# Kernel optimization log

Hardware: AMD Instinct MI355X
Metric: run time of the kernel (lower is better)

The kernel has to match this reference:

```python
import jax, jax.numpy as jnp
import numpy as np

N, E, B, PG = 20000, 320000, 20, 1000  # nodes, edges, graphs, nodes-per-graph
H, L, NB, EI = 256, 6, 16, 8           # hidden, layers, node_base_dim, edge_in_dim
LN_EPS = 1e-5


def setup_inputs() -> dict:
    key = jax.random.key(0)
    ks = jax.random.split(key, 32)
    w = lambda i, s: (jax.random.normal(ks[i], s, jnp.float32) * 0.05)
    inp = {
        "x": jax.random.normal(ks[0], (N, NB), jnp.float32),
        "edge_attr": jax.random.normal(ks[1], (E, EI), jnp.float32),
        "c": jax.random.normal(ks[2], (B, PG), jnp.float32),
        "edge_index": jax.random.randint(ks[3], (2, E), 0, N),
        "node_gid": jnp.arange(N) // PG,   # batch.batch
        "node_lid": jnp.arange(N) % PG,    # node local index
        # edge_mlp: Linear(EI,H), ReLU, Linear(H,H)
        "ew1": w(4, (EI, H)), "eb1": jnp.zeros((H,), jnp.float32),
        "ew2": w(5, (H, H)),  "eb2": jnp.zeros((H,), jnp.float32),
        # input_proj: Linear(NB+1, H), SiLU
        "in_w": w(6, (NB + 1, H)), "in_b": jnp.zeros((H,), jnp.float32),
        # per-layer GINEConv edge lin (edge_dim -> in_channels)
        "lin_w": w(7, (L, H, H)), "lin_b": jnp.zeros((L, H), jnp.float32),
        # per-layer conv MLP: Linear(H,H), SiLU, Linear(H,H)
        "cw1": w(8, (L, H, H)), "cb1": jnp.zeros((L, H), jnp.float32),
        "cw2": w(9, (L, H, H)), "cb2": jnp.zeros((L, H), jnp.float32),
        # per-layer LayerNorm
        "ln_g": jnp.ones((L, H), jnp.float32), "ln_b": jnp.zeros((L, H), jnp.float32),
        # pool_attn: Linear(H,H), Tanh, Linear(H,1)
        "pa_w1": w(10, (H, H)), "pa_b1": jnp.zeros((H,), jnp.float32),
        "pa_w2": w(11, (H, 1)), "pa_b2": jnp.zeros((1,), jnp.float32),
        # head: Linear(H,H), SiLU, Linear(H,1)
        "hw1": w(12, (H, H)), "hb1": jnp.zeros((H,), jnp.float32),
        "hw2": w(13, (H, 1)), "hb2": jnp.zeros((1,), jnp.float32),
    }
    return inp


def _layer_norm(z, g, b):
    m = jnp.mean(z, axis=-1, keepdims=True)
    v = jnp.mean(jnp.square(z - m), axis=-1, keepdims=True)
    return (z - m) * jax.lax.rsqrt(v + LN_EPS) * g + b


def reference(x, edge_attr, c, edge_index, node_gid, node_lid,
              ew1, eb1, ew2, eb2, in_w, in_b,
              lin_w, lin_b, cw1, cb1, cw2, cb2, ln_g, ln_b,
              pa_w1, pa_b1, pa_w2, pa_b2, hw1, hb1, hw2, hb2):
    silu = jax.nn.silu
    # c_scalar: per-node coefficient
    c_scalar = c[node_gid, node_lid][:, None]                       # [N,1]
    xin = jnp.concatenate([x, c_scalar], axis=-1)                   # [N,NB+1]
    e = jax.nn.relu(edge_attr @ ew1 + eb1) @ ew2 + eb2              # [E,H]
    h = silu(xin @ in_w + in_b)                                     # [N,H]
    src, dst = edge_index[0], edge_index[1]
    for l in range(L):
        msg = jax.nn.relu(h[src] + (e @ lin_w[l] + lin_b[l]))       # [E,H]
        agg = jnp.zeros_like(h).at[dst].add(msg)                    # scatter-add
        z = h + agg                                                 # (1+eps)*x_i + agg, eps=0
        h_new = silu(z @ cw1[l] + cb1[l]) @ cw2[l] + cb2[l]
        h_new = _layer_norm(h_new, ln_g[l], ln_b[l])
        h = h + silu(h_new)
    # attention pooling: global softmax over nodes, renormalized per graph
    scores = jnp.tanh(h @ pa_w1 + pa_b1) @ pa_w2 + pa_b2            # [N,1]
    attn = jax.nn.softmax(scores, axis=0)                           # [N,1]
    seg_sum = jax.ops.segment_sum(attn[:, 0], node_gid, num_segments=B)  # [B]
    attn_n = attn[:, 0] / (seg_sum[node_gid] + 1e-8)                # [N]
    pooled = jax.ops.segment_sum(h * attn_n[:, None], node_gid, num_segments=B)  # [B,H]
    q = (silu(pooled @ hw1 + hb1) @ hw2 + hb2)[:, 0]                # [B]
    return q
```

## Files before the change

### kernel.cpp

```cpp
#include <hip/hip_runtime.h>
#include <hip/hip_bf16.h>
#include <cstdint>


#define NN 20000
#define EE 320000
#define BBG 20
#define PGN 1000
#define HH 256
#define LL 6

typedef short bf16x8 __attribute__((ext_vector_type(8)));
typedef float f32x4 __attribute__((ext_vector_type(4)));

__device__ __forceinline__ void async16(const void* g, void* l) {
  __builtin_amdgcn_global_load_lds(
      (const __attribute__((address_space(1))) unsigned int*)(uintptr_t)g,
      (__attribute__((address_space(3))) unsigned int*)(uintptr_t)l, 16, 0, 0);
}

__device__ __forceinline__ float siluf(float x) { return x / (1.f + __expf(-x)); }

__device__ __forceinline__ unsigned int f2bu(float x) {
  __hip_bfloat16 h = __float2bfloat16(x);
  return (unsigned int)*(unsigned short*)&h;
}

__device__ __forceinline__ float b2f(unsigned short u) {
  unsigned int v = ((unsigned int)u) << 16;
  return *(float*)&v;
}

enum { EPI_SILU = 1, EPI_PLAIN = 2, EPI_TANH = 3 };

template <int EPI>
__global__ void __launch_bounds__(256, 2) gemm256(
    const __hip_bfloat16* __restrict__ A, const __hip_bfloat16* __restrict__ Wt,
    const float* __restrict__ bias, int M, float* __restrict__ outf,
    __hip_bfloat16* __restrict__ outb) {
  __shared__ __align__(16) __hip_bfloat16 sA[128 * 32];
  __shared__ __align__(16) __hip_bfloat16 sB[128 * 32];

  const int t = threadIdx.x;
  const int wave = t >> 6, lane = t & 63;
  const int row0 = blockIdx.x * 128;
  const int col0 = blockIdx.y * 128;

  const int wrow = (wave >> 1) * 64;
  const int wcol = (wave & 1) * 64;
  const int fr = lane & 15, q = lane >> 4;

  f32x4 zero = {0.f, 0.f, 0.f, 0.f};
  f32x4 acc[4][4];
#pragma unroll
  for (int i = 0; i < 4; i++)
#pragma unroll
    for (int j = 0; j < 4; j++) acc[i][j] = zero;

  const int c1 = t, c2 = t + 256;
  const int lr1 = c1 >> 2, lr2 = c2 >> 2;
  const int q1 = (c1 & 3) ^ ((lr1 >> 1) & 3);
  const int q2 = (c2 & 3) ^ ((lr2 >> 1) & 3);
  int rA1 = row0 + lr1; if (rA1 >= M) rA1 = M - 1;
  int rA2 = row0 + lr2; if (rA2 >= M) rA2 = M - 1;
  const int rB1 = col0 + lr1, rB2 = col0 + lr2;

  for (int k0 = 0; k0 < 256; k0 += 32) {
    async16((const char*)(A + (size_t)rA1 * HH + k0) + q1 * 16,
            (char*)sA + wave * 1024);
    async16((const char*)(A + (size_t)rA2 * HH + k0) + q2 * 16,
            (char*)sA + 4096 + wave * 1024);
    async16((const char*)(Wt + (size_t)rB1 * HH + k0) + q1 * 16,
            (char*)sB + wave * 1024);
    async16((const char*)(Wt + (size_t)rB2 * HH + k0) + q2 * 16,
            (char*)sB + 4096 + wave * 1024);
    __syncthreads();
    bf16x8 af[4], bfr[4];
#pragma unroll
    for (int i = 0; i < 4; i++) {
      const int row = wrow + i * 16 + fr;
      af[i] = *(const bf16x8*)&sA[row * 32 + ((q ^ ((row >> 1) & 3))) * 8];
    }
#pragma unroll
    for (int j = 0; j < 4; j++) {
      const int row = wcol + j * 16 + fr;
      bfr[j] = *(const bf16x8*)&sB[row * 32 + ((q ^ ((row >> 1) & 3))) * 8];
    }
#pragma unroll
    for (int i = 0; i < 4; i++)
#pragma unroll
      for (int j = 0; j < 4; j++)
        acc[i][j] = __builtin_amdgcn_mfma_f32_16x16x32_bf16(af[i], bfr[j],
                                                            acc[i][j], 0, 0, 0);
    __syncthreads();
  }

#pragma unroll
  for (int j = 0; j < 4; j++) {
    const int col = col0 + wcol + j * 16 + fr;
    const float bs = bias[col];
#pragma unroll
    for (int i = 0; i < 4; i++) {
      const int lr0 = wrow + i * 16 + q * 4;
#pragma unroll
      for (int r = 0; r < 4; r++) {
        const int grow = row0 + lr0 + r;
        float v = acc[i][j][r] + bs;
        if (grow < M) {
          if (EPI == EPI_SILU) {
            outb[(size_t)grow * HH + col] = __float2bfloat16(siluf(v));
          } else if (EPI == EPI_PLAIN) {
            outf[(size_t)grow * HH + col] = v;
          } else {
            outb[(size_t)grow * HH + col] = __float2bfloat16(tanhf(v));
          }
        }
      }
    }
  }
}

__global__ void __launch_bounds__(256, 2) gemm_silu_f32(
    const float* __restrict__ A, const __hip_bfloat16* __restrict__ Wt,
    const float* __restrict__ bias, int M, __hip_bfloat16* __restrict__ outb) {
  __shared__ __align__(16) __hip_bfloat16 sA[128 * 32];
  __shared__ __align__(16) __hip_bfloat16 sB[128 * 32];

  const int t = threadIdx.x;
  const int wave = t >> 6, lane = t & 63;
  const int row0 = blockIdx.x * 128;
  const int col0 = blockIdx.y * 128;

  const int wrow = (wave >> 1) * 64;
  const int wcol = (wave & 1) * 64;
  const int fr = lane & 15, q = lane >> 4;

  f32x4 zero = {0.f, 0.f, 0.f, 0.f};
  f32x4 acc[4][4];
#pragma unroll
  for (int i = 0; i < 4; i++)
#pragma unroll
    for (int j = 0; j < 4; j++) acc[i][j] = zero;

  const int c1 = t, c2 = t + 256;
  const int lr1 = c1 >> 2, lr2 = c2 >> 2;
  const int q1 = (c1 & 3) ^ ((lr1 >> 1) & 3);
  const int q2 = (c2 & 3) ^ ((lr2 >> 1) & 3);
  int rA1 = row0 + lr1; if (rA1 >= M) rA1 = M - 1;
  int rA2 = row0 + lr2; if (rA2 >= M) rA2 = M - 1;
  const int rB1 = col0 + lr1, rB2 = col0 + lr2;

  for (int k0 = 0; k0 < 256; k0 += 32) {
    async16((const char*)(Wt + (size_t)rB1 * HH + k0) + q1 * 16,
            (char*)sB + wave * 1024);
    async16((const char*)(Wt + (size_t)rB2 * HH + k0) + q2 * 16,
            (char*)sB + 4096 + wave * 1024);
    {
      const float* s1 = A + (size_t)rA1 * HH + k0 + q1 * 8;
      float4 a0 = *(const float4*)s1;
      float4 a1 = *(const float4*)(s1 + 4);
      uint4 u;
      u.x = f2bu(a0.x) | (f2bu(a0.y) << 16);
      u.y = f2bu(a0.z) | (f2bu(a0.w) << 16);
      u.z = f2bu(a1.x) | (f2bu(a1.y) << 16);
      u.w = f2bu(a1.z) | (f2bu(a1.w) << 16);
      *(uint4*)((char*)sA + wave * 1024 + lane * 16) = u;
    }
    {
      const float* s2 = A + (size_t)rA2 * HH + k0 + q2 * 8;
      float4 a0 = *(const float4*)s2;
      float4 a1 = *(const float4*)(s2 + 4);
      uint4 u;
      u.x = f2bu(a0.x) | (f2bu(a0.y) << 16);
      u.y = f2bu(a0.z) | (f2bu(a0.w) << 16);
      u.z = f2bu(a1.x) | (f2bu(a1.y) << 16);
      u.w = f2bu(a1.z) | (f2bu(a1.w) << 16);
      *(uint4*)((char*)sA + 4096 + wave * 1024 + lane * 16) = u;
    }
    __syncthreads();
    bf16x8 af[4], bfr[4];
#pragma unroll
    for (int i = 0; i < 4; i++) {
      const int row = wrow + i * 16 + fr;
      af[i] = *(const bf16x8*)&sA[row * 32 + ((q ^ ((row >> 1) & 3))) * 8];
    }
#pragma unroll
    for (int j = 0; j < 4; j++) {
      const int row = wcol + j * 16 + fr;
      bfr[j] = *(const bf16x8*)&sB[row * 32 + ((q ^ ((row >> 1) & 3))) * 8];
    }
#pragma unroll
    for (int i = 0; i < 4; i++)
#pragma unroll
      for (int j = 0; j < 4; j++)
        acc[i][j] = __builtin_amdgcn_mfma_f32_16x16x32_bf16(af[i], bfr[j],
                                                            acc[i][j], 0, 0, 0);
    __syncthreads();
  }

#pragma unroll
  for (int j = 0; j < 4; j++) {
    const int col = col0 + wcol + j * 16 + fr;
    const float bs = bias[col];
#pragma unroll
    for (int i = 0; i < 4; i++) {
      const int lr0 = wrow + i * 16 + q * 4;
#pragma unroll
      for (int r = 0; r < 4; r++) {
        const int grow = row0 + lr0 + r;
        if (grow < M)
          outb[(size_t)grow * HH + col] =
              __float2bfloat16(siluf(acc[i][j][r] + bs));
      }
    }
  }
}

__global__ void __launch_bounds__(256, 2) gemm_ln(
    const __hip_bfloat16* __restrict__ A, const __hip_bfloat16* __restrict__ Wt,
    const float* __restrict__ bias, const float* __restrict__ g,
    const float* __restrict__ bbv, float* __restrict__ h,
    float* __restrict__ yzf, __hip_bfloat16* __restrict__ hb) {
  __shared__ __align__(16) char smem[64 * 264 * 2];
  __hip_bfloat16* sA = (__hip_bfloat16*)smem;
  __hip_bfloat16* sB = (__hip_bfloat16*)(smem + 4096);
  unsigned short* yb = (unsigned short*)smem;

  const int t = threadIdx.x;
  const int wave = t >> 6, lane = t & 63;
  const int row0 = blockIdx.x * 64;
  const int wrow = (wave >> 1) * 32;
  const int wcol = (wave & 1) * 128;
  const int fr = lane & 15, q = lane >> 4;

  f32x4 zero = {0.f, 0.f, 0.f, 0.f};
  f32x4 acc[2][8];
#pragma unroll
  for (int i = 0; i < 2; i++)
#pragma unroll
    for (int j = 0; j < 8; j++) acc[i][j] = zero;

  const int lrA = t >> 2;
  const int qA = (t & 3) ^ ((lrA >> 1) & 3);
  int rA = row0 + lrA; if (rA >= NN) rA = NN - 1;
  int qB[4], rB[4];
#pragma unroll
  for (int p = 0; p < 4; p++) {
    const int c = t + p * 256;
    const int lr = c >> 2;
    qB[p] = (c & 3) ^ ((lr >> 1) & 3);
    rB[p] = lr;
  }

  for (int k0 = 0; k0 < 256; k0 += 32) {
    async16((const char*)(A + (size_t)rA * HH + k0) + qA * 16,
            (char*)sA + wave * 1024);
#pragma unroll
    for (int p = 0; p < 4; p++)
      async16((const char*)(Wt + (size_t)rB[p] * HH + k0) + qB[p] * 16,
              (char*)sB + p * 4096 + wave * 1024);
    __syncthreads();
    bf16x8 af[2], bfr[8];
#pragma unroll
    for (int i = 0; i < 2; i++) {
      const int row = wrow + i * 16 + fr;
      af[i] = *(const bf16x8*)&sA[row * 32 + ((q ^ ((row >> 1) & 3))) * 8];
    }
#pragma unroll
    for (int j = 0; j < 8; j++) {
      const int row = wcol + j * 16 + fr;
      bfr[j] = *(const bf16x8*)&sB[row * 32 + ((q ^ ((row >> 1) & 3))) * 8];
    }
#pragma unroll
    for (int i = 0; i < 2; i++)
#pragma unroll
      for (int j = 0; j < 8; j++)
        acc[i][j] = __builtin_amdgcn_mfma_f32_16x16x32_bf16(af[i], bfr[j],
                                                            acc[i][j], 0, 0, 0);
    __syncthreads();
  }

#pragma unroll
  for (int j = 0; j < 8; j++) {
    const int col = wcol + j * 16 + fr;
    const float bs = bias[col];
#pragma unroll
    for (int i = 0; i < 2; i++) {
      const int r0 = wrow + i * 16 + q * 4;
#pragma unroll
      for (int r = 0; r < 4; r++)
        yb[(r0 + r) * 264 + col] = (unsigned short)f2bu(acc[i][j][r] + bs);
    }
  }
  __syncthreads();

  for (int rr = 0; rr < 16; rr++) {
    const int r = wave * 16 + rr;
    const int grow = row0 + r;
    if (grow >= NN) break;
    float v[4];
    float s = 0.f;
#pragma unroll
    for (int i = 0; i < 4; i++) {
      v[i] = b2f(yb[r * 264 + lane + i * 64]);
      s += v[i];
    }
#pragma unroll
    for (int o = 32; o; o >>= 1) s += __shfl_xor(s, o);
    const float mean = s * (1.f / 256.f);
    float var = 0.f;
#pragma unroll
    for (int i = 0; i < 4; i++) { float d = v[i] - mean; var += d * d; }
#pragma unroll
    for (int o = 32; o; o >>= 1) var += __shfl_xor(var, o);
    const float rs = rsqrtf(var * (1.f / 256.f) + 1e-5f);
#pragma unroll
    for (int i = 0; i < 4; i++) {
      const int c = lane + i * 64;
      float ln = (v[i] - mean) * rs * g[c] + bbv[c];
      float si = siluf(ln);
      size_t idx = (size_t)grow * HH + c;
      float nh = h[idx] + si;
      h[idx] = nh;
      yzf[idx] = nh;
      hb[idx] = __float2bfloat16(nh);
    }
  }
}

__global__ void __launch_bounds__(256, 3) edge_fused(
    const __hip_bfloat16* __restrict__ te, const __hip_bfloat16* __restrict__ Wt,
    const float* __restrict__ bias, const __hip_bfloat16* __restrict__ hbv,
    const int* __restrict__ srcp, const int* __restrict__ dstp,
    float* __restrict__ z) {
  __shared__ __align__(16) char smem[32768];
  __shared__ int sSrc[128], sDst[128];
  __hip_bfloat16* sA = (__hip_bfloat16*)smem;
  __hip_bfloat16* sB = (__hip_bfloat16*)(smem + 16384);
  unsigned short* sRed = (unsigned short*)smem;

  const int t = threadIdx.x;
  const int wave = t >> 6, lane = t & 63;
  const int row0 = blockIdx.y * 128;
  const int col0 = blockIdx.x * 128;

  if (t < 128) { sSrc[t] = srcp[row0 + t]; sDst[t] = dstp[row0 + t]; }
  __syncthreads();

  const int wrow = (wave >> 1) * 64;
  const int fr = lane & 15, q = lane >> 4;
  const int rc = lane, rb = wave;

  f32x4 zero = {0.f, 0.f, 0.f, 0.f};
  f32x4 acc[4][4];
#pragma unroll
  for (int i = 0; i < 4; i++)
#pragma unroll
    for (int j = 0; j < 4; j++) acc[i][j] = zero;

  const int c1 = t, c2 = t + 256;
  const int lr1 = c1 >> 2, lr2 = c2 >> 2;
  const int q1 = (c1 & 3) ^ ((lr1 >> 1) & 3);
  const int q2 = (c2 & 3) ^ ((lr2 >> 1) & 3);
  const int rA1 = row0 + lr1, rA2 = row0 + lr2;
  const int rB1 = col0 + lr1, rB2 = col0 + lr2;

  float hv[32];

#pragma unroll
  for (int it = 0; it < 4; it++) {
    const int ka = it * 64, kb = ka + 32;
    async16((const char*)(te + (size_t)rA1 * HH + ka) + q1 * 16,
            (char*)sA + wave * 1024);
    async16((const char*)(te + (size_t)rA2 * HH + ka) + q2 * 16,
            (char*)sA + 4096 + wave * 1024);
    async16((const char*)(te + (size_t)rA1 * HH + kb) + q1 * 16,
            (char*)sA + 8192 + wave * 1024);
    async16((const char*)(te + (size_t)rA2 * HH + kb) + q2 * 16,
            (char*)sA + 12288 + wave * 1024);
    async16((const char*)(Wt + (size_t)rB1 * HH + ka) + q1 * 16,
            (char*)sB + wave * 1024);
    async16((const char*)(Wt + (size_t)rB2 * HH + ka) + q2 * 16,
            (char*)sB + 4096 + wave * 1024);
    async16((const char*)(Wt + (size_t)rB1 * HH + kb) + q1 * 16,
            (char*)sB + 8192 + wave * 1024);
    async16((const char*)(Wt + (size_t)rB2 * HH + kb) + q2 * 16,
            (char*)sB + 12288 + wave * 1024);
#pragma unroll
    for (int u = 0; u < 8; u++) {
      const int r = it * 8 + u;
      hv[r] = __bfloat162float(hbv[(size_t)sSrc[rb * 32 + r] * HH + col0 + rc]);
    }
    __syncthreads();
#pragma unroll
    for (int half = 0; half < 2; half++) {
      const __hip_bfloat16* pA = sA + half * 4096;
      const __hip_bfloat16* pB = sB + half * 4096;
      bf16x8 af[4], bfr[4];
#pragma unroll
      for (int i = 0; i < 4; i++) {
        const int row = wrow + i * 16 + fr;
        af[i] = *(const bf16x8*)&pA[row * 32 + ((q ^ ((row >> 1) & 3))) * 8];
      }
#pragma unroll
      for (int j = 0; j < 4; j++) {
        const int row = (wave & 1) * 64 + j * 16 + fr;
        bfr[j] = *(const bf16x8*)&pB[row * 32 + ((q ^ ((row >> 1) & 3))) * 8];
      }
#pragma unroll
      for (int i = 0; i < 4; i++)
#pragma unroll
        for (int j = 0; j < 4; j++)
          acc[i][j] = __builtin_amdgcn_mfma_f32_16x16x32_bf16(af[i], bfr[j],
                                                              acc[i][j], 0, 0, 0);
    }
    __syncthreads();
  }

#pragma unroll
  for (int hf = 0; hf < 2; hf++) {
    if ((wave & 1) == hf) {
#pragma unroll
      for (int j = 0; j < 4; j++) {
        const int cl = j * 16 + fr;
        const float bs = bias[col0 + hf * 64 + cl];
#pragma unroll
        for (int i = 0; i < 4; i++) {
          const int r0 = wrow + i * 16 + q * 4;
          f32x4 v = acc[i][j];
          unsigned int p0 = f2bu(v[0] + bs) | (f2bu(v[1] + bs) << 16);
          unsigned int p1 = f2bu(v[2] + bs) | (f2bu(v[3] + bs) << 16);
          *(unsigned int*)&sRed[cl * 130 + r0] = p0;
          *(unsigned int*)&sRed[cl * 130 + r0 + 2] = p1;
        }
      }
    }
    __syncthreads();
    const int gcol = col0 + hf * 64 + rc;
    float a = 0.f;
    int cur = sDst[rb * 32];
#pragma unroll 4
    for (int rr = 0; rr < 32; rr++) {
      const int row = rb * 32 + rr;
      const int d = sDst[row];
      if (d != cur) {
        unsafeAtomicAdd(&z[(size_t)cur * HH + gcol], a);
        a = 0.f;
        cur = d;
      }
      float m = b2f(sRed[rc * 130 + row]) + hv[rr];
      a += m > 0.f ? m : 0.f;
    }
    unsafeAtomicAdd(&z[(size_t)cur * HH + gcol], a);
    if (hf == 0) {
#pragma unroll
      for (int rr = 0; rr < 32; rr++)
        hv[rr] = __bfloat162float(
            hbv[(size_t)sSrc[rb * 32 + rr] * HH + col0 + 64 + rc]);
    }
    __syncthreads();
  }
}

__global__ void __launch_bounds__(256) hist_k(const int* __restrict__ edst,
                                              int* __restrict__ cnt) {
  const int e = blockIdx.x * 256 + threadIdx.x;
  if (e < EE) atomicAdd(&cnt[edst[e]], 1);
}

__global__ void __launch_bounds__(256) scan_k(const int* __restrict__ cnt,
                                              int* __restrict__ rowptr) {
  __shared__ int buf[256];
  __shared__ int carry;
  const int t = threadIdx.x;
  if (t == 0) carry = 0;
  __syncthreads();
  for (int base = 0; base < NN; base += 256) {
    const int idx = base + t;
    int v = (idx < NN) ? cnt[idx] : 0;
    buf[t] = v;
    __syncthreads();
    for (int o = 1; o < 256; o <<= 1) {
      int x = (t >= o) ? buf[t - o] : 0;
      __syncthreads();
      buf[t] += x;
      __syncthreads();
    }
    if (idx < NN) rowptr[idx] = carry + buf[t] - v;
    __syncthreads();
    if (t == 255) carry += buf[255];
    __syncthreads();
  }
  if (t == 0) rowptr[NN] = carry;
}

__global__ void __launch_bounds__(256) scatter_k(
    const int* __restrict__ esrc, const int* __restrict__ edst,
    int* __restrict__ cursor, int* __restrict__ posof,
    int* __restrict__ srcp, int* __restrict__ dstp) {
  const int e = blockIdx.x * 256 + threadIdx.x;
  if (e < EE) {
    const int d = edst[e];
    const int pos = atomicAdd(&cursor[d], 1);
    posof[e] = pos;
    srcp[pos] = esrc[e];
    dstp[pos] = d;
  }
}

__global__ void __launch_bounds__(256) edge_hidden(
    const float* __restrict__ ea, const float* __restrict__ ew1,
    const float* __restrict__ eb1, const int* __restrict__ posof,
    __hip_bfloat16* __restrict__ tout) {
  __shared__ float w[8 * 256];
  __shared__ float b[256];
  __shared__ float sea[16 * 8];
  __shared__ int spos[16];
  const int t = threadIdx.x;
  for (int i = t; i < 8 * 256; i += 256) w[i] = ew1[i];
  b[t] = eb1[t];
  const int e0 = blockIdx.x * 16;
  if (t < 128) sea[t] = ea[(size_t)e0 * 8 + t];
  if (t < 16) spos[t] = posof[e0 + t];
  __syncthreads();
  for (int e = 0; e < 16; e++) {
    float a = b[t];
#pragma unroll
    for (int j = 0; j < 8; j++) a += sea[e * 8 + j] * w[j * 256 + t];
    tout[(size_t)spos[e] * HH + t] = __float2bfloat16(a > 0.f ? a : 0.f);
  }
}

__global__ void __launch_bounds__(256) fold_edge_w(
    const float* __restrict__ ew2, const float* __restrict__ lin_w,
    const float* __restrict__ eb2, const float* __restrict__ lin_b,
    __hip_bfloat16* __restrict__ Wlt, float* __restrict__ bl) {
  const int l = blockIdx.x >> 8, j = blockIdx.x & 255;
  const int c = threadIdx.x;
  __shared__ float row[256];
  row[c] = ew2[j * 256 + c];
  __syncthreads();
  const float* lw = lin_w + (size_t)l * 65536;
  float a = 0.f;
  for (int k = 0; k < 256; k++) a += row[k] * lw[k * 256 + c];
  Wlt[((size_t)l * 256 + c) * 256 + j] = __float2bfloat16(a);
  if (j == 0) {
    float s = lin_b[l * 256 + c];
    for (int k = 0; k < 256; k++) s += eb2[k] * lw[k * 256 + c];
    bl[l * 256 + c] = s;
  }
}

__global__ void __launch_bounds__(256) tcast_all(
    const float* __restrict__ cw1, const float* __restrict__ cw2,
    const float* __restrict__ paw1, __hip_bfloat16* __restrict__ cw1t,
    __hip_bfloat16* __restrict__ cw2t, __hip_bfloat16* __restrict__ paw1t) {
  const int b = blockIdx.x;
  const float* s;
  __hip_bfloat16* d;
  if (b < 1536) { int l = b >> 8; s = cw1 + (size_t)l * 65536; d = cw1t + (size_t)l * 65536; }
  else if (b < 3072) { int l = (b - 1536) >> 8; s = cw2 + (size_t)l * 65536; d = cw2t + (size_t)l * 65536; }
  else { s = paw1; d = paw1t; }
  const int r = b & 255, c = threadIdx.x;
  d[(size_t)c * 256 + r] = __float2bfloat16(s[(size_t)r * 256 + c]);
}

__global__ void __launch_bounds__(256) node_init(
    const float* __restrict__ x, const float* __restrict__ cc,
    const int* __restrict__ gid, const int* __restrict__ lid,
    const float* __restrict__ in_w, const float* __restrict__ in_b,
    float* __restrict__ h, float* __restrict__ yzf,
    __hip_bfloat16* __restrict__ hb) {
  __shared__ float w[17 * 256];
  __shared__ float b[256];
  __shared__ float sx[16 * 17];
  const int t = threadIdx.x;
  for (int i = t; i < 17 * 256; i += 256) w[i] = in_w[i];
  b[t] = in_b[t];
  const int n0 = blockIdx.x * 16;
  sx[(t >> 4) * 17 + (t & 15)] = x[(size_t)(n0 + (t >> 4)) * 16 + (t & 15)];
  if (t < 16) {
    int n = n0 + t;
    sx[t * 17 + 16] = cc[gid[n] * PGN + lid[n]];
  }
  __syncthreads();
  for (int e = 0; e < 16; e++) {
    float a = b[t];
#pragma unroll
    for (int j = 0; j < 17; j++) a += sx[e * 17 + j] * w[j * 256 + t];
    float s = siluf(a);
    size_t idx = (size_t)(n0 + e) * HH + t;
    h[idx] = s;
    yzf[idx] = s;
    hb[idx] = __float2bfloat16(s);
  }
}

__global__ void __launch_bounds__(256) score_k(
    const __hip_bfloat16* __restrict__ s1, const float* __restrict__ pw2,
    const float* __restrict__ pb2, float* __restrict__ scores,
    float* __restrict__ pmax) {
  __shared__ float w2[256];
  __shared__ float bm[4];
  const int t = threadIdx.x, wave = t >> 6, lane = t & 63;
  w2[t] = pw2[t];
  __syncthreads();
  const size_t row = (size_t)blockIdx.x * 4 + wave;
  float a = 0.f;
#pragma unroll
  for (int i = 0; i < 4; i++) {
    int c = lane + i * 64;
    a += __bfloat162float(s1[row * HH + c]) * w2[c];
  }
#pragma unroll
  for (int o = 32; o; o >>= 1) a += __shfl_xor(a, o);
  float sc = a + pb2[0];
  if (lane == 0) { scores[row] = sc; bm[wave] = sc; }
  __syncthreads();
  if (t == 0) pmax[blockIdx.x] = fmaxf(fmaxf(bm[0], bm[1]), fmaxf(bm[2], bm[3]));
}

__global__ void __launch_bounds__(256) gmax_k(const float* __restrict__ pmax,
                                              int n, float* __restrict__ gmax) {
  const int t = threadIdx.x;
  float m = -3.4e38f;
  for (int i = t; i < n; i += 256) m = fmaxf(m, pmax[i]);
#pragma unroll
  for (int o = 32; o; o >>= 1) m = fmaxf(m, __shfl_xor(m, o));
  __shared__ float wm[4];
  if ((t & 63) == 0) wm[t >> 6] = m;
  __syncthreads();
  if (t == 0) gmax[0] = fmaxf(fmaxf(wm[0], wm[1]), fmaxf(wm[2], wm[3]));
}

__global__ void __launch_bounds__(256) esum_k(
    const float* __restrict__ scores, const int* __restrict__ gid,
    const float* __restrict__ gmax, float* __restrict__ en,
    float* __restrict__ seg) {
  __shared__ float ls[BBG + 1];
  const int t = threadIdx.x;
  if (t < BBG + 1) ls[t] = 0.f;
  __syncthreads();
  const int n = blockIdx.x * 256 + t;
  if (n < NN) {
    float e = __expf(scores[n] - gmax[0]);
    en[n] = e;
    atomicAdd(&ls[gid[n]], e);
    atomicAdd(&ls[BBG], e);
  }
  __syncthreads();
  if (t < BBG + 1) unsafeAtomicAdd(&seg[t], ls[t]);
}

__global__ void __launch_bounds__(256) pooled_k(
    const float* __restrict__ h, const float* __restrict__ en,
    const float* __restrict__ seg, float* __restrict__ pooled) {
  const int g = blockIdx.x / 40, ch = blockIdx.x % 40;
  const int c = threadIdx.x;
  const int n0 = g * PGN + ch * 25;
  float a = 0.f;
  for (int i = 0; i < 25; i++) {
    int n = n0 + i;
    a += en[n] * h[(size_t)n * HH + c];
  }
  const float inv = 1.f / (seg[g] + 1e-8f * seg[BBG]);
  unsafeAtomicAdd(&pooled[g * HH + c], a * inv);
}

__global__ void __launch_bounds__(256) head_k(
    const float* __restrict__ pooled, const float* __restrict__ hw1,
    const float* __restrict__ hb1, const float* __restrict__ hw2,
    const float* __restrict__ hb2, float* __restrict__ qout) {
  const int b = blockIdx.x, c = threadIdx.x;
  __shared__ float p[256];
  __shared__ float wsum[4];
  p[c] = pooled[b * 256 + c];
  __syncthreads();
  float a = hb1[c];
  for (int k = 0; k < 256; k++) a += p[k] * hw1[k * 256 + c];
  float v = siluf(a) * hw2[c];
#pragma unroll
  for (int o = 32; o; o >>= 1) v += __shfl_xor(v, o);
  if ((c & 63) == 0) wsum[c >> 6] = v;
  __syncthreads();
  if (c == 0) qout[b] = wsum[0] + wsum[1] + wsum[2] + wsum[3] + hb2[0];
}

extern "C" void kernel_launch(void* const* d_in, const int* in_sizes, int n_in,
                              void* d_out, int out_size, void* d_ws, size_t ws_size,
                              hipStream_t stream) {
  const float* x = (const float*)d_in[0];
  const float* edge_attr = (const float*)d_in[1];
  const float* cc = (const float*)d_in[2];
  const int* edge_index = (const int*)d_in[3];
  const int* node_gid = (const int*)d_in[4];
  const int* node_lid = (const int*)d_in[5];
  const float* ew1 = (const float*)d_in[6];
  const float* eb1 = (const float*)d_in[7];
  const float* ew2 = (const float*)d_in[8];
  const float* eb2 = (const float*)d_in[9];
  const float* in_w = (const float*)d_in[10];
  const float* in_b = (const float*)d_in[11];
  const float* lin_w = (const float*)d_in[12];
  const float* lin_b = (const float*)d_in[13];
  const float* cw1 = (const float*)d_in[14];
  const float* cb1 = (const float*)d_in[15];
  const float* cw2 = (const float*)d_in[16];
  const float* cb2 = (const float*)d_in[17];
  const float* ln_g = (const float*)d_in[18];
  const float* ln_b = (const float*)d_in[19];
  const float* pa_w1 = (const float*)d_in[20];
  const float* pa_b1 = (const float*)d_in[21];
  const float* pa_w2 = (const float*)d_in[22];
  const float* pa_b2 = (const float*)d_in[23];
  const float* hw1 = (const float*)d_in[24];
  const float* hb1 = (const float*)d_in[25];
  const float* hw2 = (const float*)d_in[26];
  const float* hb2 = (const float*)d_in[27];
  float* qout = (float*)d_out;

  char* w = (char*)d_ws;
  auto alloc = [&](size_t bytes) {
    char* p = w;
    w += (bytes + 255) & ~(size_t)255;
    return p;
  };
  __hip_bfloat16* t_e = (__hip_bfloat16*)alloc((size_t)EE * HH * 2);
  float* h = (float*)alloc((size_t)NN * HH * 4);
  float* yzf = (float*)alloc((size_t)NN * HH * 4);
  __hip_bfloat16* hb = (__hip_bfloat16*)alloc((size_t)NN * HH * 2);
  __hip_bfloat16* t2 = (__hip_bfloat16*)alloc((size_t)NN * HH * 2);
  __hip_bfloat16* Wlt = (__hip_bfloat16*)alloc((size_t)LL * HH * HH * 2);
  float* bl = (float*)alloc((size_t)LL * HH * 4);
  __hip_bfloat16* cw1t = (__hip_bfloat16*)alloc((size_t)LL * HH * HH * 2);
  __hip_bfloat16* cw2t = (__hip_bfloat16*)alloc((size_t)LL * HH * HH * 2);
  __hip_bfloat16* paw1t = (__hip_bfloat16*)alloc((size_t)HH * HH * 2);
  float* scores = (float*)alloc((size_t)NN * 4);
  float* pmax = (float*)alloc(5008 * 4);
  float* en = (float*)alloc((size_t)NN * 4);
  float* seg = (float*)alloc((BBG + 1) * 4);
  float* gmax = (float*)alloc(4);
  float* pooled = (float*)alloc((size_t)BBG * HH * 4);
  int* cnt = (int*)alloc((size_t)NN * 4);
  int* rowptr = (int*)alloc((size_t)(NN + 1) * 4);
  int* cursor = (int*)alloc((size_t)NN * 4);
  int* posof = (int*)alloc((size_t)EE * 4);
  int* srcp = (int*)alloc((size_t)EE * 4);
  int* dstp = (int*)alloc((size_t)EE * 4);

  const int* esrc = edge_index;
  const int* edst = edge_index + EE;

  hipMemsetAsync(cnt, 0, (size_t)NN * 4, stream);
  hipMemsetAsync(seg, 0, (BBG + 1) * 4, stream);
  hipMemsetAsync(pooled, 0, (size_t)BBG * HH * 4, stream);

  hist_k<<<(EE + 255) / 256, 256, 0, stream>>>(edst, cnt);
  scan_k<<<1, 256, 0, stream>>>(cnt, rowptr);
  hipMemcpyAsync(cursor, rowptr, (size_t)NN * 4, hipMemcpyDeviceToDevice, stream);
  scatter_k<<<(EE + 255) / 256, 256, 0, stream>>>(esrc, edst, cursor, posof,
                                                  srcp, dstp);

  fold_edge_w<<<LL * 256, 256, 0, stream>>>(ew2, lin_w, eb2, lin_b, Wlt, bl);
  tcast_all<<<3328, 256, 0, stream>>>(cw1, cw2, pa_w1, cw1t, cw2t, paw1t);
  edge_hidden<<<EE / 16, 256, 0, stream>>>(edge_attr, ew1, eb1, posof, t_e);
  node_init<<<NN / 16, 256, 0, stream>>>(x, cc, node_gid, node_lid, in_w, in_b,
                                         h, yzf, hb);

  dim3 gE(2, EE / 128), gN((NN + 127) / 128, 2);
  const int gLN = (NN + 63) / 64;
  for (int l = 0; l < LL; l++) {
    edge_fused<<<gE, 256, 0, stream>>>(t_e, Wlt + (size_t)l * HH * HH,
                                       bl + l * HH, hb, srcp, dstp, yzf);
    gemm_silu_f32<<<gN, 256, 0, stream>>>(
        yzf, cw1t + (size_t)l * HH * HH, cb1 + l * HH, NN, t2);
    gemm_ln<<<gLN, 256, 0, stream>>>(t2, cw2t + (size_t)l * HH * HH,
                                     cb2 + l * HH, ln_g + l * HH, ln_b + l * HH,
                                     h, yzf, hb);
  }

  gemm256<EPI_TANH><<<gN, 256, 0, stream>>>(hb, paw1t, pa_b1, NN, nullptr, t2);
  score_k<<<NN / 4, 256, 0, stream>>>(t2, pa_w2, pa_b2, scores, pmax);
  gmax_k<<<1, 256, 0, stream>>>(pmax, NN / 4, gmax);
  esum_k<<<(NN + 255) / 256, 256, 0, stream>>>(scores, node_gid, gmax, en, seg);
  pooled_k<<<BBG * 40, 256, 0, stream>>>(h, en, seg, pooled);
  head_k<<<BBG, 256, 0, stream>>>(pooled, hw1, hb1, hw2, hb2, qout);
}
```

Measured before the change: 1.377 ms.

## Recompute edge hidden features inside edge kernel instead of materializing them

Drops the precomputed [E,256] bf16 edge-hidden tensor. Each edge_fused block now rebuilds its A tile on the fly from the 8-wide raw edge attributes and ew1/eb1 held in shared memory, so every layer avoids reading a large buffer from global memory. In exchange, each block redoes the small 8-input matmul plus ReLU for every layer and column block, and shared-memory use and register pressure in the hot kernel go up. Separately, the one-block prefix scan now uses wave shuffles in place of a shared-memory Hillis-Steele loop with many barriers.

```diff
diff --git a/kernel.cpp b/kernel.cpp
--- a/kernel.cpp
+++ b/kernel.cpp
@@ -329,11 +329,14 @@
 }
 
 __global__ void __launch_bounds__(256, 3) edge_fused(
-    const __hip_bfloat16* __restrict__ te, const __hip_bfloat16* __restrict__ Wt,
-    const float* __restrict__ bias, const __hip_bfloat16* __restrict__ hbv,
-    const int* __restrict__ srcp, const int* __restrict__ dstp,
-    float* __restrict__ z) {
+    const float* __restrict__ ea, const int* __restrict__ eorig,
+    const float* __restrict__ ew1f, const float* __restrict__ eb1f,
+    const __hip_bfloat16* __restrict__ Wt, const float* __restrict__ bias,
+    const __hip_bfloat16* __restrict__ hbv, const int* __restrict__ srcp,
+    const int* __restrict__ dstp, float* __restrict__ z) {
   __shared__ __align__(16) char smem[32768];
+  __shared__ __align__(16) float sew1[8 * 256];
+  __shared__ float seb1[256];
   __shared__ int sSrc[128], sDst[128];
   __hip_bfloat16* sA = (__hip_bfloat16*)smem;
   __hip_bfloat16* sB = (__hip_bfloat16*)(smem + 16384);
@@ -345,11 +348,26 @@
   const int col0 = blockIdx.x * 128;
 
   if (t < 128) { sSrc[t] = srcp[row0 + t]; sDst[t] = dstp[row0 + t]; }
-  __syncthreads();
+  for (int i = t; i < 8 * 256; i += 256) sew1[i] = ew1f[i];
+  seb1[t] = eb1f[t];
+
+  const int rr = (t >> 3) * 4;
+  const int cc = (t & 7) * 4;
+  float ar[4][8];
+#pragma unroll
+  for (int i = 0; i < 4; i++) {
+    const int e = eorig[row0 + rr + i];
+    const float4 a0 = *(const float4*)&ea[(size_t)e * 8];
+    const float4 a1 = *(const float4*)&ea[(size_t)e * 8 + 4];
+    ar[i][0] = a0.x; ar[i][1] = a0.y; ar[i][2] = a0.z; ar[i][3] = a0.w;
+    ar[i][4] = a1.x; ar[i][5] = a1.y; ar[i][6] = a1.z; ar[i][7] = a1.w;
+  }
 
   const int wrow = (wave >> 1) * 64;
   const int fr = lane & 15, q = lane >> 4;
   const int rc = lane, rb = wave;
+  const int gch = cc >> 3;
+  const int hby = (cc & 7) * 2;
 
   f32x4 zero = {0.f, 0.f, 0.f, 0.f};
   f32x4 acc[4][4];
@@ -362,22 +380,15 @@
   const int lr1 = c1 >> 2, lr2 = c2 >> 2;
   const int q1 = (c1 & 3) ^ ((lr1 >> 1) & 3);
   const int q2 = (c2 & 3) ^ ((lr2 >> 1) & 3);
-  const int rA1 = row0 + lr1, rA2 = row0 + lr2;
   const int rB1 = col0 + lr1, rB2 = col0 + lr2;
 
   float hv[32];
+
+  __syncthreads();
 
 #pragma unroll
   for (int it = 0; it < 4; it++) {
     const int ka = it * 64, kb = ka + 32;
-    async16((const char*)(te + (size_t)rA1 * HH + ka) + q1 * 16,
-            (char*)sA + wave * 1024);
-    async16((const char*)(te + (size_t)rA2 * HH + ka) + q2 * 16,
-            (char*)sA + 4096 + wave * 1024);
-    async16((const char*)(te + (size_t)rA1 * HH + kb) + q1 * 16,
-            (char*)sA + 8192 + wave * 1024);
-    async16((const char*)(te + (size_t)rA2 * HH + kb) + q2 * 16,
-            (char*)sA + 12288 + wave * 1024);
     async16((const char*)(Wt + (size_t)rB1 * HH + ka) + q1 * 16,
             (char*)sB + wave * 1024);
     async16((const char*)(Wt + (size_t)rB2 * HH + ka) + q2 * 16,
@@ -386,6 +397,38 @@
             (char*)sB + 8192 + wave * 1024);
     async16((const char*)(Wt + (size_t)rB2 * HH + kb) + q2 * 16,
             (char*)sB + 12288 + wave * 1024);
+#pragma unroll
+    for (int half = 0; half < 2; half++) {
+      const int k0 = ka + half * 32;
+      float tv[4][4];
+      const float4 bb = *(const float4*)&seb1[k0 + cc];
+#pragma unroll
+      for (int i = 0; i < 4; i++) {
+        tv[i][0] = bb.x; tv[i][1] = bb.y; tv[i][2] = bb.z; tv[i][3] = bb.w;
+      }
+#pragma unroll
+      for (int j = 0; j < 8; j++) {
+        const float4 ww = *(const float4*)&sew1[j * 256 + k0 + cc];
+#pragma unroll
+        for (int i = 0; i < 4; i++) {
+          tv[i][0] += ar[i][j] * ww.x;
+          tv[i][1] += ar[i][j] * ww.y;
+          tv[i][2] += ar[i][j] * ww.z;
+          tv[i][3] += ar[i][j] * ww.w;
+        }
+      }
+#pragma unroll
+      for (int i = 0; i < 4; i++) {
+        const int r = rr + i;
+        const int sl = gch ^ ((r >> 1) & 3);
+        ushort4 pk;
+        pk.x = (unsigned short)f2bu(tv[i][0] > 0.f ? tv[i][0] : 0.f);
+        pk.y = (unsigned short)f2bu(tv[i][1] > 0.f ? tv[i][1] : 0.f);
+        pk.z = (unsigned short)f2bu(tv[i][2] > 0.f ? tv[i][2] : 0.f);
+        pk.w = (unsigned short)f2bu(tv[i][3] > 0.f ? tv[i][3] : 0.f);
+        *(ushort4*)((char*)sA + half * 8192 + r * 64 + sl * 16 + hby) = pk;
+      }
+    }
 #pragma unroll
     for (int u = 0; u < 8; u++) {
       const int r = it * 8 + u;
@@ -440,23 +483,23 @@
     float a = 0.f;
     int cur = sDst[rb * 32];
 #pragma unroll 4
-    for (int rr = 0; rr < 32; rr++) {
-      const int row = rb * 32 + rr;
+    for (int r2 = 0; r2 < 32; r2++) {
+      const int row = rb * 32 + r2;
       const int d = sDst[row];
       if (d != cur) {
         unsafeAtomicAdd(&z[(size_t)cur * HH + gcol], a);
         a = 0.f;
         cur = d;
       }
-      float m = b2f(sRed[rc * 130 + row]) + hv[rr];
+      float m = b2f(sRed[rc * 130 + row]) + hv[r2];
       a += m > 0.f ? m : 0.f;
     }
     unsafeAtomicAdd(&z[(size_t)cur * HH + gcol], a);
     if (hf == 0) {
 #pragma unroll
-      for (int rr = 0; rr < 32; rr++)
-        hv[rr] = __bfloat162float(
-            hbv[(size_t)sSrc[rb * 32 + rr] * HH + col0 + 64 + rc]);
+      for (int r2 = 0; r2 < 32; r2++)
+        hv[r2] = __bfloat162float(
+            hbv[(size_t)sSrc[rb * 32 + r2] * HH + col0 + 64 + rc]);
     }
     __syncthreads();
   }
@@ -470,25 +513,28 @@
 
 __global__ void __launch_bounds__(256) scan_k(const int* __restrict__ cnt,
                                               int* __restrict__ rowptr) {
-  __shared__ int buf[256];
+  __shared__ int wsum[4];
   __shared__ int carry;
-  const int t = threadIdx.x;
+  const int t = threadIdx.x, wave = t >> 6, lane = t & 63;
   if (t == 0) carry = 0;
   __syncthreads();
   for (int base = 0; base < NN; base += 256) {
     const int idx = base + t;
     int v = (idx < NN) ? cnt[idx] : 0;
-    buf[t] = v;
-    __syncthreads();
-    for (int o = 1; o < 256; o <<= 1) {
-      int x = (t >= o) ? buf[t - o] : 0;
-      __syncthreads();
-      buf[t] += x;
-      __syncthreads();
-    }
-    if (idx < NN) rowptr[idx] = carry + buf[t] - v;
-    __syncthreads();
-    if (t == 255) carry += buf[255];
+    int inc = v;
+#pragma unroll
+    for (int o = 1; o < 64; o <<= 1) {
+      int u = __shfl_up(inc, o);
+      if (lane >= o) inc += u;
+    }
+    if (lane == 63) wsum[wave] = inc;
+    __syncthreads();
+    int woff = 0;
+    for (int w2 = 0; w2 < wave; w2++) woff += wsum[w2];
+    if (idx < NN) rowptr[idx] = carry + woff + inc - v;
+    const int total = wsum[0] + wsum[1] + wsum[2] + wsum[3];
+    __syncthreads();
+    if (t == 0) carry += total;
     __syncthreads();
   }
   if (t == 0) rowptr[NN] = carry;
@@ -496,38 +542,15 @@
 
 __global__ void __launch_bounds__(256) scatter_k(
     const int* __restrict__ esrc, const int* __restrict__ edst,
-    int* __restrict__ cursor, int* __restrict__ posof,
+    int* __restrict__ cursor, int* __restrict__ eorig,
     int* __restrict__ srcp, int* __restrict__ dstp) {
   const int e = blockIdx.x * 256 + threadIdx.x;
   if (e < EE) {
     const int d = edst[e];
     const int pos = atomicAdd(&cursor[d], 1);
-    posof[e] = pos;
+    eorig[pos] = e;
     srcp[pos] = esrc[e];
     dstp[pos] = d;
-  }
-}
-
-__global__ void __launch_bounds__(256) edge_hidden(
-    const float* __restrict__ ea, const float* __restrict__ ew1,
-    const float* __restrict__ eb1, const int* __restrict__ posof,
-    __hip_bfloat16* __restrict__ tout) {
-  __shared__ float w[8 * 256];
-  __shared__ float b[256];
-  __shared__ float sea[16 * 8];
-  __shared__ int spos[16];
-  const int t = threadIdx.x;
-  for (int i = t; i < 8 * 256; i += 256) w[i] = ew1[i];
-  b[t] = eb1[t];
-  const int e0 = blockIdx.x * 16;
-  if (t < 128) sea[t] = ea[(size_t)e0 * 8 + t];
-  if (t < 16) spos[t] = posof[e0 + t];
-  __syncthreads();
-  for (int e = 0; e < 16; e++) {
-    float a = b[t];
-#pragma unroll
-    for (int j = 0; j < 8; j++) a += sea[e * 8 + j] * w[j * 256 + t];
-    tout[(size_t)spos[e] * HH + t] = __float2bfloat16(a > 0.f ? a : 0.f);
   }
 }
 
@@ -725,7 +748,6 @@
     w += (bytes + 255) & ~(size_t)255;
     return p;
   };
-  __hip_bfloat16* t_e = (__hip_bfloat16*)alloc((size_t)EE * HH * 2);
   float* h = (float*)alloc((size_t)NN * HH * 4);
   float* yzf = (float*)alloc((size_t)NN * HH * 4);
   __hip_bfloat16* hb = (__hip_bfloat16*)alloc((size_t)NN * HH * 2);
@@ -744,7 +766,7 @@
   int* cnt = (int*)alloc((size_t)NN * 4);
   int* rowptr = (int*)alloc((size_t)(NN + 1) * 4);
   int* cursor = (int*)alloc((size_t)NN * 4);
-  int* posof = (int*)alloc((size_t)EE * 4);
+  int* eorig = (int*)alloc((size_t)EE * 4);
   int* srcp = (int*)alloc((size_t)EE * 4);
   int* dstp = (int*)alloc((size_t)EE * 4);
 
@@ -758,20 +780,20 @@
   hist_k<<<(EE + 255) / 256, 256, 0, stream>>>(edst, cnt);
   scan_k<<<1, 256, 0, stream>>>(cnt, rowptr);
   hipMemcpyAsync(cursor, rowptr, (size_t)NN * 4, hipMemcpyDeviceToDevice, stream);
-  scatter_k<<<(EE + 255) / 256, 256, 0, stream>>>(esrc, edst, cursor, posof,
+  scatter_k<<<(EE + 255) / 256, 256, 0, stream>>>(esrc, edst, cursor, eorig,
                                                   srcp, dstp);
 
   fold_edge_w<<<LL * 256, 256, 0, stream>>>(ew2, lin_w, eb2, lin_b, Wlt, bl);
   tcast_all<<<3328, 256, 0, stream>>>(cw1, cw2, pa_w1, cw1t, cw2t, paw1t);
-  edge_hidden<<<EE / 16, 256, 0, stream>>>(edge_attr, ew1, eb1, posof, t_e);
   node_init<<<NN / 16, 256, 0, stream>>>(x, cc, node_gid, node_lid, in_w, in_b,
                                          h, yzf, hb);
 
   dim3 gE(2, EE / 128), gN((NN + 127) / 128, 2);
   const int gLN = (NN + 63) / 64;
   for (int l = 0; l < LL; l++) {
-    edge_fused<<<gE, 256, 0, stream>>>(t_e, Wlt + (size_t)l * HH * HH,
-                                       bl + l * HH, hb, srcp, dstp, yzf);
+    edge_fused<<<gE, 256, 0, stream>>>(edge_attr, eorig, ew1, eb1,
+                                       Wlt + (size_t)l * HH * HH, bl + l * HH,
+                                       hb, srcp, dstp, yzf);
     gemm_silu_f32<<<gN, 256, 0, stream>>>(
         yzf, cw1t + (size_t)l * HH * HH, cb1 + l * HH, NN, t2);
     gemm_ln<<<gLN, 256, 0, stream>>>(t2, cw2t + (size_t)l * HH * HH,
```

New measurement: 1.808 ms. 31.3% more time.

## Fuse conv MLP GEMMs with LayerNorm and restructure edge gather and scan

Applied to the files above, without the earlier changes.

Merges the two per-layer conv MLP GEMMs and the LayerNorm into one kernel. The SiLU intermediate for each 64-row tile stays in shared memory as bf16 instead of going through global memory. The edge kernel now gathers h[src] in chunks of 8 just before accumulation rather than holding a 32-float register array, and its launch bound rises to 4 blocks. The single-block scan switches to wave shuffles. The fused kernel uses more shared memory and gives each wave all 256 columns, which may lower occupancy and reuse.

```diff
diff --git a/kernel.cpp b/kernel.cpp
--- a/kernel.cpp
+++ b/kernel.cpp
@@ -120,43 +120,43 @@
   }
 }
 
-__global__ void __launch_bounds__(256, 2) gemm_silu_f32(
-    const float* __restrict__ A, const __hip_bfloat16* __restrict__ Wt,
-    const float* __restrict__ bias, int M, __hip_bfloat16* __restrict__ outb) {
-  __shared__ __align__(16) __hip_bfloat16 sA[128 * 32];
-  __shared__ __align__(16) __hip_bfloat16 sB[128 * 32];
+__global__ void __launch_bounds__(256, 2) mlp_ln(
+    const float* __restrict__ z, const __hip_bfloat16* __restrict__ W1t,
+    const float* __restrict__ b1, const __hip_bfloat16* __restrict__ W2t,
+    const float* __restrict__ b2, const float* __restrict__ g,
+    const float* __restrict__ bbv, float* __restrict__ h,
+    float* __restrict__ yzf, __hip_bfloat16* __restrict__ hb) {
+  __shared__ __align__(16) char smem[20480 + 64 * 264 * 2];
+  __hip_bfloat16* sA = (__hip_bfloat16*)smem;
+  __hip_bfloat16* sB = (__hip_bfloat16*)(smem + 4096);
+  unsigned short* sT = (unsigned short*)(smem + 20480);
 
   const int t = threadIdx.x;
   const int wave = t >> 6, lane = t & 63;
-  const int row0 = blockIdx.x * 128;
-  const int col0 = blockIdx.y * 128;
-
-  const int wrow = (wave >> 1) * 64;
-  const int wcol = (wave & 1) * 64;
+  const int row0 = blockIdx.x * 64;
   const int fr = lane & 15, q = lane >> 4;
+  const int wr = wave * 16;
+
+  const int lrA = t >> 2;
+  const int qA = (t & 3) ^ ((lrA >> 1) & 3);
+  int rA = row0 + lrA; if (rA >= NN) rA = NN - 1;
+  int qB[4], rB[4];
+#pragma unroll
+  for (int p = 0; p < 4; p++) {
+    const int c = t + p * 256;
+    const int lr = c >> 2;
+    qB[p] = (c & 3) ^ ((lr >> 1) & 3);
+    rB[p] = lr;
+  }
 
   f32x4 zero = {0.f, 0.f, 0.f, 0.f};
-  f32x4 acc[4][4];
-#pragma unroll
-  for (int i = 0; i < 4; i++)
-#pragma unroll
-    for (int j = 0; j < 4; j++) acc[i][j] = zero;
-
-  const int c1 = t, c2 = t + 256;
-  const int lr1 = c1 >> 2, lr2 = c2 >> 2;
-  const int q1 = (c1 & 3) ^ ((lr1 >> 1) & 3);
-  const int q2 = (c2 & 3) ^ ((lr2 >> 1) & 3);
-  int rA1 = row0 + lr1; if (rA1 >= M) rA1 = M - 1;
-  int rA2 = row0 + lr2; if (rA2 >= M) rA2 = M - 1;
-  const int rB1 = col0 + lr1, rB2 = col0 + lr2;
+  f32x4 acc[16];
+#pragma unroll
+  for (int j = 0; j < 16; j++) acc[j] = zero;
 
   for (int k0 = 0; k0 < 256; k0 += 32) {
-    async16((const char*)(Wt + (size_t)rB1 * HH + k0) + q1 * 16,
-            (char*)sB + wave * 1024);
-    async16((const char*)(Wt + (size_t)rB2 * HH + k0) + q2 * 16,
-            (char*)sB + 4096 + wave * 1024);
     {
-      const float* s1 = A + (size_t)rA1 * HH + k0 + q1 * 8;
+      const float* s1 = z + (size_t)rA * HH + k0 + qA * 8;
       float4 a0 = *(const float4*)s1;
       float4 a1 = *(const float4*)(s1 + 4);
       uint4 u;
@@ -164,145 +164,74 @@
       u.y = f2bu(a0.z) | (f2bu(a0.w) << 16);
       u.z = f2bu(a1.x) | (f2bu(a1.y) << 16);
       u.w = f2bu(a1.z) | (f2bu(a1.w) << 16);
-      *(uint4*)((char*)sA + wave * 1024 + lane * 16) = u;
-    }
+      *(uint4*)((char*)sA + t * 16) = u;
+    }
+#pragma unroll
+    for (int p = 0; p < 4; p++)
+      async16((const char*)(W1t + (size_t)rB[p] * HH + k0) + qB[p] * 16,
+              (char*)sB + p * 4096 + wave * 1024);
+    __syncthreads();
+    bf16x8 af;
     {
-      const float* s2 = A + (size_t)rA2 * HH + k0 + q2 * 8;
-      float4 a0 = *(const float4*)s2;
-      float4 a1 = *(const float4*)(s2 + 4);
-      uint4 u;
-      u.x = f2bu(a0.x) | (f2bu(a0.y) << 16);
-      u.y = f2bu(a0.z) | (f2bu(a0.w) << 16);
-      u.z = f2bu(a1.x) | (f2bu(a1.y) << 16);
-      u.w = f2bu(a1.z) | (f2bu(a1.w) << 16);
-      *(uint4*)((char*)sA + 4096 + wave * 1024 + lane * 16) = u;
-    }
-    __syncthreads();
-    bf16x8 af[4], bfr[4];
-#pragma unroll
-    for (int i = 0; i < 4; i++) {
-      const int row = wrow + i * 16 + fr;
-      af[i] = *(const bf16x8*)&sA[row * 32 + ((q ^ ((row >> 1) & 3))) * 8];
-    }
-#pragma unroll
-    for (int j = 0; j < 4; j++) {
-      const int row = wcol + j * 16 + fr;
-      bfr[j] = *(const bf16x8*)&sB[row * 32 + ((q ^ ((row >> 1) & 3))) * 8];
-    }
-#pragma unroll
-    for (int i = 0; i < 4; i++)
-#pragma unroll
-      for (int j = 0; j < 4; j++)
-        acc[i][j] = __builtin_amdgcn_mfma_f32_16x16x32_bf16(af[i], bfr[j],
-                                                            acc[i][j], 0, 0, 0);
-    __syncthreads();
-  }
-
-#pragma unroll
-  for (int j = 0; j < 4; j++) {
-    const int col = col0 + wcol + j * 16 + fr;
-    const float bs = bias[col];
-#pragma unroll
-    for (int i = 0; i < 4; i++) {
-      const int lr0 = wrow + i * 16 + q * 4;
-#pragma unroll
-      for (int r = 0; r < 4; r++) {
-        const int grow = row0 + lr0 + r;
-        if (grow < M)
-          outb[(size_t)grow * HH + col] =
-              __float2bfloat16(siluf(acc[i][j][r] + bs));
-      }
-    }
-  }
-}
-
-__global__ void __launch_bounds__(256, 2) gemm_ln(
-    const __hip_bfloat16* __restrict__ A, const __hip_bfloat16* __restrict__ Wt,
-    const float* __restrict__ bias, const float* __restrict__ g,
-    const float* __restrict__ bbv, float* __restrict__ h,
-    float* __restrict__ yzf, __hip_bfloat16* __restrict__ hb) {
-  __shared__ __align__(16) char smem[64 * 264 * 2];
-  __hip_bfloat16* sA = (__hip_bfloat16*)smem;
-  __hip_bfloat16* sB = (__hip_bfloat16*)(smem + 4096);
-  unsigned short* yb = (unsigned short*)smem;
-
-  const int t = threadIdx.x;
-  const int wave = t >> 6, lane = t & 63;
-  const int row0 = blockIdx.x * 64;
-  const int wrow = (wave >> 1) * 32;
-  const int wcol = (wave & 1) * 128;
-  const int fr = lane & 15, q = lane >> 4;
-
-  f32x4 zero = {0.f, 0.f, 0.f, 0.f};
-  f32x4 acc[2][8];
-#pragma unroll
-  for (int i = 0; i < 2; i++)
-#pragma unroll
-    for (int j = 0; j < 8; j++) acc[i][j] = zero;
-
-  const int lrA = t >> 2;
-  const int qA = (t & 3) ^ ((lrA >> 1) & 3);
-  int rA = row0 + lrA; if (rA >= NN) rA = NN - 1;
-  int qB[4], rB[4];
-#pragma unroll
-  for (int p = 0; p < 4; p++) {
-    const int c = t + p * 256;
-    const int lr = c >> 2;
-    qB[p] = (c & 3) ^ ((lr >> 1) & 3);
-    rB[p] = lr;
-  }
+      const int row = wr + fr;
+      af = *(const bf16x8*)&sA[row * 32 + ((q ^ ((row >> 1) & 3))) * 8];
+    }
+#pragma unroll
+    for (int j = 0; j < 16; j++) {
+      const int row = j * 16 + fr;
+      bf16x8 bfr = *(const bf16x8*)&sB[row * 32 + ((q ^ ((row >> 1) & 3))) * 8];
+      acc[j] = __builtin_amdgcn_mfma_f32_16x16x32_bf16(af, bfr, acc[j], 0, 0, 0);
+    }
+    __syncthreads();
+  }
+#pragma unroll
+  for (int j = 0; j < 16; j++) {
+    const int col = j * 16 + fr;
+    const float bs = b1[col];
+    const int r0 = wr + q * 4;
+#pragma unroll
+    for (int r = 0; r < 4; r++)
+      sT[(r0 + r) * 264 + col] =
+          (unsigned short)f2bu(siluf(acc[j][r] + bs));
+  }
+#pragma unroll
+  for (int j = 0; j < 16; j++) acc[j] = zero;
 
   for (int k0 = 0; k0 < 256; k0 += 32) {
-    async16((const char*)(A + (size_t)rA * HH + k0) + qA * 16,
-            (char*)sA + wave * 1024);
 #pragma unroll
     for (int p = 0; p < 4; p++)
-      async16((const char*)(Wt + (size_t)rB[p] * HH + k0) + qB[p] * 16,
+      async16((const char*)(W2t + (size_t)rB[p] * HH + k0) + qB[p] * 16,
               (char*)sB + p * 4096 + wave * 1024);
     __syncthreads();
-    bf16x8 af[2], bfr[8];
-#pragma unroll
-    for (int i = 0; i < 2; i++) {
-      const int row = wrow + i * 16 + fr;
-      af[i] = *(const bf16x8*)&sA[row * 32 + ((q ^ ((row >> 1) & 3))) * 8];
-    }
-#pragma unroll
-    for (int j = 0; j < 8; j++) {
-      const int row = wcol + j * 16 + fr;
-      bfr[j] = *(const bf16x8*)&sB[row * 32 + ((q ^ ((row >> 1) & 3))) * 8];
-    }
-#pragma unroll
-    for (int i = 0; i < 2; i++)
-#pragma unroll
-      for (int j = 0; j < 8; j++)
-        acc[i][j] = __builtin_amdgcn_mfma_f32_16x16x32_bf16(af[i], bfr[j],
-                                                            acc[i][j], 0, 0, 0);
-    __syncthreads();
-  }
-
-#pragma unroll
-  for (int j = 0; j < 8; j++) {
-    const int col = wcol + j * 16 + fr;
-    const float bs = bias[col];
-#pragma unroll
-    for (int i = 0; i < 2; i++) {
-      const int r0 = wrow + i * 16 + q * 4;
-#pragma unroll
-      for (int r = 0; r < 4; r++)
-        yb[(r0 + r) * 264 + col] = (unsigned short)f2bu(acc[i][j][r] + bs);
-    }
+    bf16x8 af = *(const bf16x8*)&sT[(wr + fr) * 264 + k0 + q * 8];
+#pragma unroll
+    for (int j = 0; j < 16; j++) {
+      const int row = j * 16 + fr;
+      bf16x8 bfr = *(const bf16x8*)&sB[row * 32 + ((q ^ ((row >> 1) & 3))) * 8];
+      acc[j] = __builtin_amdgcn_mfma_f32_16x16x32_bf16(af, bfr, acc[j], 0, 0, 0);
+    }
+    __syncthreads();
+  }
+#pragma unroll
+  for (int j = 0; j < 16; j++) {
+    const int col = j * 16 + fr;
+    const float bs = b2[col];
+    const int r0 = wr + q * 4;
+#pragma unroll
+    for (int r = 0; r < 4; r++)
+      sT[(r0 + r) * 264 + col] = (unsigned short)f2bu(acc[j][r] + bs);
   }
   __syncthreads();
 
   for (int rr = 0; rr < 16; rr++) {
-    const int r = wave * 16 + rr;
+    const int r = wr + rr;
     const int grow = row0 + r;
     if (grow >= NN) break;
     float v[4];
     float s = 0.f;
 #pragma unroll
     for (int i = 0; i < 4; i++) {
-      v[i] = b2f(yb[r * 264 + lane + i * 64]);
+      v[i] = b2f(sT[r * 264 + lane + i * 64]);
       s += v[i];
     }
 #pragma unroll
@@ -328,7 +257,7 @@
   }
 }
 
-__global__ void __launch_bounds__(256, 3) edge_fused(
+__global__ void __launch_bounds__(256, 4) edge_fused(
     const __hip_bfloat16* __restrict__ te, const __hip_bfloat16* __restrict__ Wt,
     const float* __restrict__ bias, const __hip_bfloat16* __restrict__ hbv,
     const int* __restrict__ srcp, const int* __restrict__ dstp,
@@ -364,8 +293,6 @@
   const int q2 = (c2 & 3) ^ ((lr2 >> 1) & 3);
   const int rA1 = row0 + lr1, rA2 = row0 + lr2;
   const int rB1 = col0 + lr1, rB2 = col0 + lr2;
-
-  float hv[32];
 
 #pragma unroll
   for (int it = 0; it < 4; it++) {
@@ -386,11 +313,6 @@
             (char*)sB + 8192 + wave * 1024);
     async16((const char*)(Wt + (size_t)rB2 * HH + kb) + q2 * 16,
             (char*)sB + 12288 + wave * 1024);
-#pragma unroll
-    for (int u = 0; u < 8; u++) {
-      const int r = it * 8 + u;
-      hv[r] = __bfloat162float(hbv[(size_t)sSrc[rb * 32 + r] * HH + col0 + rc]);
-    }
     __syncthreads();
 #pragma unroll
     for (int half = 0; half < 2; half++) {
@@ -439,25 +361,26 @@
     const int gcol = col0 + hf * 64 + rc;
     float a = 0.f;
     int cur = sDst[rb * 32];
-#pragma unroll 4
-    for (int rr = 0; rr < 32; rr++) {
-      const int row = rb * 32 + rr;
-      const int d = sDst[row];
-      if (d != cur) {
-        unsafeAtomicAdd(&z[(size_t)cur * HH + gcol], a);
-        a = 0.f;
-        cur = d;
+    for (int ch = 0; ch < 4; ch++) {
+      float hv8[8];
+#pragma unroll
+      for (int u = 0; u < 8; u++)
+        hv8[u] = __bfloat162float(
+            hbv[(size_t)sSrc[rb * 32 + ch * 8 + u] * HH + gcol]);
+#pragma unroll
+      for (int u = 0; u < 8; u++) {
+        const int row = rb * 32 + ch * 8 + u;
+        const int d = sDst[row];
+        if (d != cur) {
+          unsafeAtomicAdd(&z[(size_t)cur * HH + gcol], a);
+          a = 0.f;
+          cur = d;
+        }
+        float m = b2f(sRed[rc * 130 + row]) + hv8[u];
+        a += m > 0.f ? m : 0.f;
       }
-      float m = b2f(sRed[rc * 130 + row]) + hv[rr];
-      a += m > 0.f ? m : 0.f;
     }
     unsafeAtomicAdd(&z[(size_t)cur * HH + gcol], a);
-    if (hf == 0) {
-#pragma unroll
-      for (int rr = 0; rr < 32; rr++)
-        hv[rr] = __bfloat162float(
-            hbv[(size_t)sSrc[rb * 32 + rr] * HH + col0 + 64 + rc]);
-    }
     __syncthreads();
   }
 }
@@ -470,25 +393,28 @@
 
 __global__ void __launch_bounds__(256) scan_k(const int* __restrict__ cnt,
                                               int* __restrict__ rowptr) {
-  __shared__ int buf[256];
+  __shared__ int wsum[4];
   __shared__ int carry;
-  const int t = threadIdx.x;
+  const int t = threadIdx.x, wave = t >> 6, lane = t & 63;
   if (t == 0) carry = 0;
   __syncthreads();
   for (int base = 0; base < NN; base += 256) {
     const int idx = base + t;
     int v = (idx < NN) ? cnt[idx] : 0;
-    buf[t] = v;
-    __syncthreads();
-    for (int o = 1; o < 256; o <<= 1) {
-      int x = (t >= o) ? buf[t - o] : 0;
-      __syncthreads();
-      buf[t] += x;
-      __syncthreads();
-    }
-    if (idx < NN) rowptr[idx] = carry + buf[t] - v;
-    __syncthreads();
-    if (t == 255) carry += buf[255];
+    int inc = v;
+#pragma unroll
+    for (int o = 1; o < 64; o <<= 1) {
+      int u = __shfl_up(inc, o);
+      if (lane >= o) inc += u;
+    }
+    if (lane == 63) wsum[wave] = inc;
+    __syncthreads();
+    int woff = 0;
+    for (int w2 = 0; w2 < wave; w2++) woff += wsum[w2];
+    if (idx < NN) rowptr[idx] = carry + woff + inc - v;
+    const int total = wsum[0] + wsum[1] + wsum[2] + wsum[3];
+    __syncthreads();
+    if (t == 0) carry += total;
     __syncthreads();
   }
   if (t == 0) rowptr[NN] = carry;
@@ -768,15 +694,14 @@
                                          h, yzf, hb);
 
   dim3 gE(2, EE / 128), gN((NN + 127) / 128, 2);
-  const int gLN = (NN + 63) / 64;
+  const int gMLP = (NN + 63) / 64;
   for (int l = 0; l < LL; l++) {
     edge_fused<<<gE, 256, 0, stream>>>(t_e, Wlt + (size_t)l * HH * HH,
                                        bl + l * HH, hb, srcp, dstp, yzf);
-    gemm_silu_f32<<<gN, 256, 0, stream>>>(
-        yzf, cw1t + (size_t)l * HH * HH, cb1 + l * HH, NN, t2);
-    gemm_ln<<<gLN, 256, 0, stream>>>(t2, cw2t + (size_t)l * HH * HH,
-                                     cb2 + l * HH, ln_g + l * HH, ln_b + l * HH,
-                                     h, yzf, hb);
+    mlp_ln<<<gMLP, 256, 0, stream>>>(
+        yzf, cw1t + (size_t)l * HH * HH, cb1 + l * HH,
+        cw2t + (size_t)l * HH * HH, cb2 + l * HH, ln_g + l * HH, ln_b + l * HH,
+        h, yzf, hb);
   }
 
   gemm256<EPI_TANH><<<gN, 256, 0, stream>>>(hb, paw1t, pa_b1, NN, nullptr, t2);
```

Measured after the change: 1.207 ms. 12.3% less time.
